# Kernel tuning notes

Hardware: AMD Instinct MI355X
Metric: run time of the kernel (lower is better)

## Reference

```python
import jax, jax.numpy as jnp
import numpy as np

ALPHA = 0.1
K = 10


def setup_inputs() -> dict:
    key = jax.random.key(0)
    k1, k2, k3, k4, k5, k6 = jax.random.split(key, 6)
    N, F_in, H = 100000, 256, 128
    E, E_lp = 1600000, 400000
    return {
        "x": jax.random.normal(k1, (N, F_in), dtype=jnp.float32),
        "edge_index": jax.random.randint(k2, (2, E), 0, N, dtype=jnp.int64),
        "pos_edge_index": jax.random.randint(k3, (2, E_lp), 0, N, dtype=jnp.int64),
        "neg_edge_index": jax.random.randint(k4, (2, E_lp), 0, N, dtype=jnp.int64),
        "W1": jax.random.normal(k5, (F_in, H), dtype=jnp.float32) * (1.0 / np.sqrt(F_in)),
        "W2": jax.random.normal(k6, (H, H), dtype=jnp.float32) * (1.0 / np.sqrt(H)),
    }


def _appnp_propagate(h, src, dst, norm, num_nodes):
    # z_{k+1} = (1-alpha) * A_hat z_k + alpha * h   (K hops)
    z = h
    for _ in range(K):
        msg = norm[:, None] * z[src]                         # [E+N, d] gather
        agg = jax.ops.segment_sum(msg, dst, num_segments=num_nodes)  # scatter-add
        z = (1.0 - ALPHA) * agg + ALPHA * h
    return z


def reference(x, edge_index, pos_edge_index, neg_edge_index, W1, W2):
    N = x.shape[0]
    # add self-loops, GCN symmetric normalization: d^-1/2 A_sl d^-1/2
    loops = jnp.arange(N, dtype=edge_index.dtype)
    src = jnp.concatenate([edge_index[0], loops])
    dst = jnp.concatenate([edge_index[1], loops])
    deg = jax.ops.segment_sum(jnp.ones_like(dst, dtype=x.dtype), dst, num_segments=N)
    dinv = jax.lax.rsqrt(jnp.maximum(deg, 1.0))
    norm = dinv[src] * dinv[dst]

    # encode: two APPNP layers with ReLU in between (drop_rate = 0)
    z = _appnp_propagate(x @ W1, src, dst, norm, N)
    z = jax.nn.relu(z)
    z = _appnp_propagate(z @ W2, src, dst, norm, N)

    # decode: edge dot products over concatenated pos/neg edges
    e = jnp.concatenate([pos_edge_index, neg_edge_index], axis=-1)
    return jnp.sum(z[e[0]] * z[e[1]], axis=-1)
```

## Files before the change

kernel.cpp:

```cpp
#include <hip/hip_runtime.h>


constexpr int Hd = 128;
constexpr int Fin = 256;
constexpr float A_ = 0.1f;
constexpr float OMA = 0.9f;

typedef float vf2 __attribute__((ext_vector_type(2)));
typedef __bf16 bf16x8 __attribute__((ext_vector_type(8)));
typedef float f32x4 __attribute__((ext_vector_type(4)));

__device__ __forceinline__ int idx_at(const void* p, size_t i, int is64) {
    if (is64) return (int)((const long long*)p)[i];
    return ((const int*)p)[i];
}

__device__ __forceinline__ unsigned short bf16_of(float x) {
    unsigned u = __float_as_uint(x);
    return (unsigned short)((u + 0x7fffu + ((u >> 16) & 1u)) >> 16);
}

__device__ __forceinline__ unsigned pack_bf16x2(float x, float y) {
    unsigned ux = __float_as_uint(x);
    unsigned uy = __float_as_uint(y);
    ux = (ux + 0x7fffu + ((ux >> 16) & 1u)) >> 16;
    uy = (uy + 0x7fffu + ((uy >> 16) & 1u)) & 0xffff0000u;
    return ux | uy;
}

__device__ __forceinline__ float2 unpack_bf16x2(unsigned v) {
    float2 r;
    r.x = __uint_as_float(v << 16);
    r.y = __uint_as_float(v & 0xffff0000u);
    return r;
}

__device__ __forceinline__ unsigned short pack_fp8x2(float x, float y) {
    int v = __builtin_amdgcn_cvt_pk_fp8_f32(x, y, 0, false);
    return (unsigned short)(unsigned)v;
}

__device__ __forceinline__ float2 unpack_fp8x2(unsigned short v) {
    vf2 r = __builtin_amdgcn_cvt_pk_f32_fp8((int)(unsigned)v, false);
    float2 o;
    o.x = r[0];
    o.y = r[1];
    return o;
}

__global__ void k_detect(const int* __restrict__ p, int npairs, int* __restrict__ flag) {
    __shared__ int any32;
    if (threadIdx.x == 0) any32 = 0;
    __syncthreads();
    for (int i = threadIdx.x; i < npairs; i += blockDim.x)
        if (p[2 * i + 1] != 0) any32 = 1;
    __syncthreads();
    if (threadIdx.x == 0) *flag = any32 ? 0 : 1;
}


__global__ void k_zero_i32(int* __restrict__ p, int n) {
    int i = blockIdx.x * blockDim.x + threadIdx.x;
    if (i < n) p[i] = 0;
}

__global__ void k_count(const void* __restrict__ ei, int E, int* __restrict__ cnt,
                        const int* __restrict__ flag) {
    int is64 = *flag;
    int e = blockIdx.x * blockDim.x + threadIdx.x;
    if (e < E) {
        int d = idx_at(ei, (size_t)E + e, is64);
        atomicAdd(&cnt[d], 1);
    }
}

__global__ void k_dinv(const int* __restrict__ cnt, float* __restrict__ dinv, int N) {
    int i = blockIdx.x * blockDim.x + threadIdx.x;
    if (i < N) dinv[i] = rsqrtf((float)(cnt[i] + 1));
}

__global__ void k_scan1(const int* __restrict__ cnt, int* __restrict__ rp,
                        int* __restrict__ bsum, int N) {
    __shared__ int s[256];
    int t = threadIdx.x;
    int i = blockIdx.x * 256 + t;
    int v = (i < N) ? (cnt[i] + 1) : 0;
    s[t] = v;
    __syncthreads();
    for (int off = 1; off < 256; off <<= 1) {
        int add = (t >= off) ? s[t - off] : 0;
        __syncthreads();
        s[t] += add;
        __syncthreads();
    }
    if (i < N) rp[i] = s[t] - v;
    if (t == 255) bsum[blockIdx.x] = s[255];
}

__global__ void k_scan2(int* __restrict__ bsum, int nb) {
    __shared__ int s[512];
    int t = threadIdx.x;
    int v = (t < nb) ? bsum[t] : 0;
    s[t] = v;
    __syncthreads();
    for (int off = 1; off < 512; off <<= 1) {
        int add = (t >= off) ? s[t - off] : 0;
        __syncthreads();
        s[t] += add;
        __syncthreads();
    }
    if (t < nb) bsum[t] = s[t] - v;
}

__global__ void k_scan3(int* __restrict__ rp, const int* __restrict__ bsum,
                        int* __restrict__ cursor, int* __restrict__ col,
                        int N, int Etot) {
    int i = blockIdx.x * blockDim.x + threadIdx.x;
    if (i < N) {
        int r = rp[i] + bsum[i >> 8];
        rp[i] = r;
        cursor[i] = 1;
        col[r] = i;
    }
    if (i == 0) rp[N] = Etot;
}

__global__ __launch_bounds__(256) void k_place(const void* __restrict__ ei, int E,
                                               const int* __restrict__ rp,
                                               int* __restrict__ cursor,
                                               int* __restrict__ col,
                                               const int* __restrict__ flag) {
    const int is64 = *flag;
    const int e0 = (blockIdx.x * blockDim.x + threadIdx.x) * 4;
    if (e0 >= E) return;
    const int n = min(4, E - e0);
    int s[4], d[4];
#pragma unroll
    for (int k = 0; k < 4; ++k) {
        int e = e0 + min(k, n - 1);
        s[k] = idx_at(ei, (size_t)e, is64);
        d[k] = idx_at(ei, (size_t)E + e, is64);
    }
    int pos[4];
#pragma unroll
    for (int k = 0; k < 4; ++k)
        if (k < n) pos[k] = rp[d[k]] + atomicAdd(&cursor[d[k]], 1);
#pragma unroll
    for (int k = 0; k < 4; ++k)
        if (k < n) col[pos[k]] = s[k];
}

__global__ void k_wt(const float* __restrict__ W, unsigned short* __restrict__ Wt, int K) {
    int i = blockIdx.x * blockDim.x + threadIdx.x;
    if (i < K * 128) {
        int k = i >> 7, c = i & 127;
        Wt[c * K + k] = bf16_of(W[i]);
    }
}


template <int KTOT, bool AF32>
__global__ __launch_bounds__(256) void k_gemm_mfma(const void* __restrict__ Ap,
                                                   const unsigned short* __restrict__ Wt,
                                                   const float* __restrict__ dinv,
                                                   unsigned short* __restrict__ z0,
                                                   unsigned* __restrict__ ah, int N) {
    __shared__ __align__(16) char smem[64 * 132 * 4];
    unsigned short (*As)[40] = (unsigned short(*)[40])smem;
    unsigned short (*Bs)[40] = (unsigned short(*)[40])(smem + 5120);
    float (*Cs)[132] = (float(*)[132])smem;

    const int t    = threadIdx.x;
    const int lane = t & 63;
    const int w    = t >> 6;
    const int wr   = w >> 1;
    const int wc   = w & 1;
    const int r0   = blockIdx.x * 64;

    f32x4 acc[2][4];
#pragma unroll
    for (int i = 0; i < 2; ++i)
#pragma unroll
        for (int j = 0; j < 4; ++j)
#pragma unroll
            for (int q = 0; q < 4; ++q) acc[i][j][q] = 0.f;

    const int arow = t >> 2;
    const int akc  = (t & 3) * 8;
    const int bcol = t >> 1;
    const int bkc  = (t & 1) * 16;

    for (int k0 = 0; k0 < KTOT; k0 += 32) {
        {
            int gr = r0 + arow;
            if (AF32) {
                uint4 s = make_uint4(0, 0, 0, 0);
                if (gr < N) {
                    const float* a = (const float*)Ap + (size_t)gr * KTOT + k0 + akc;
                    float4 v0 = *(const float4*)a;
                    float4 v1 = *(const float4*)(a + 4);
                    s.x = pack_bf16x2(v0.x, v0.y);
                    s.y = pack_bf16x2(v0.z, v0.w);
                    s.z = pack_bf16x2(v1.x, v1.y);
                    s.w = pack_bf16x2(v1.z, v1.w);
                }
                *(uint4*)&As[arow][akc] = s;
            } else {
                uint4 s = make_uint4(0, 0, 0, 0);
                if (gr < N) s = *(const uint4*)((const unsigned short*)Ap + (size_t)gr * KTOT + k0 + akc);
                *(uint4*)&As[arow][akc] = s;
            }
        }
        {
            const unsigned short* wsrc = Wt + (size_t)bcol * KTOT + k0 + bkc;
            *(uint4*)&Bs[bcol][bkc]     = *(const uint4*)wsrc;
            *(uint4*)&Bs[bcol][bkc + 8] = *(const uint4*)(wsrc + 8);
        }
        __syncthreads();
        {
            const int kblk = (lane >> 4) * 8;
            const int l15  = lane & 15;
            bf16x8 af[2], bfr[4];
#pragma unroll
            for (int i = 0; i < 2; ++i)
                af[i] = *(const bf16x8*)&As[wr * 32 + i * 16 + l15][kblk];
#pragma unroll
            for (int j = 0; j < 4; ++j)
                bfr[j] = *(const bf16x8*)&Bs[wc * 64 + j * 16 + l15][kblk];
#pragma unroll
            for (int i = 0; i < 2; ++i)
#pragma unroll
                for (int j = 0; j < 4; ++j)
                    acc[i][j] = __builtin_amdgcn_mfma_f32_16x16x32_bf16(af[i], bfr[j], acc[i][j], 0, 0, 0);
        }
        __syncthreads();
    }

    {
        const int l15 = lane & 15;
        const int rq  = (lane >> 4) * 4;
#pragma unroll
        for (int i = 0; i < 2; ++i)
#pragma unroll
            for (int j = 0; j < 4; ++j)
#pragma unroll
                for (int q = 0; q < 4; ++q)
                    Cs[wr * 32 + i * 16 + rq + q][wc * 64 + j * 16 + l15] = acc[i][j][q];
    }
    __syncthreads();
    {
        const int row = t >> 2;
        const int cb  = (t & 3) * 32;
        const int gr  = r0 + row;
        if (gr < N) {
            float dv = dinv[gr];
            float c[32];
#pragma unroll
            for (int m = 0; m < 8; ++m) {
                float4 v = *(const float4*)&Cs[row][cb + m * 4];
                c[m * 4 + 0] = v.x; c[m * 4 + 1] = v.y; c[m * 4 + 2] = v.z; c[m * 4 + 3] = v.w;
            }
            unsigned pk[8];
#pragma unroll
            for (int m = 0; m < 8; ++m) {
                unsigned lo = (unsigned)pack_fp8x2(dv * c[4 * m + 0], dv * c[4 * m + 1]);
                unsigned hi = (unsigned)pack_fp8x2(dv * c[4 * m + 2], dv * c[4 * m + 3]);
                pk[m] = lo | (hi << 16);
            }
            uint4* zd = (uint4*)&z0[((size_t)gr << 6) + (cb >> 1)];
            zd[0] = make_uint4(pk[0], pk[1], pk[2], pk[3]);
            zd[1] = make_uint4(pk[4], pk[5], pk[6], pk[7]);
            unsigned am[16];
#pragma unroll
            for (int m = 0; m < 16; ++m)
                am[m] = pack_bf16x2(A_ * c[2 * m], A_ * c[2 * m + 1]);
            uint4* ad = (uint4*)&ah[((size_t)gr << 6) + (cb >> 1)];
            ad[0] = make_uint4(am[0],  am[1],  am[2],  am[3]);
            ad[1] = make_uint4(am[4],  am[5],  am[6],  am[7]);
            ad[2] = make_uint4(am[8],  am[9],  am[10], am[11]);
            ad[3] = make_uint4(am[12], am[13], am[14], am[15]);
        }
    }
}


template <int B>
__device__ __forceinline__ void hop_batch(const unsigned short* __restrict__ yb,
                                          const int* __restrict__ col,
                                          int e, int lane,
                                          float& ax, float& ay,
                                          float& bx, float& by) {
    int c[B];
#pragma unroll
    for (int k = 0; k < B; ++k) c[k] = col[e + k];
    unsigned short v[B];
#pragma unroll
    for (int k = 0; k < B; ++k) v[k] = yb[((unsigned)c[k] << 6) + lane];
#pragma unroll
    for (int k = 0; k < B; ++k) {
        float2 z = unpack_fp8x2(v[k]);
        if (k & 1) { bx += z.x; by += z.y; }
        else       { ax += z.x; ay += z.y; }
    }
}

template <int OUTM>
__global__ __launch_bounds__(256) void k_hop(const unsigned short* __restrict__ yin,
                                             const unsigned* __restrict__ ah,
                                             const float* __restrict__ dinv,
                                             void* __restrict__ zout,
                                             const int* __restrict__ rp,
                                             const int* __restrict__ col, int N) {
    int wid  = (blockIdx.x * blockDim.x + threadIdx.x) >> 6;
    int lane = threadIdx.x & 63;
    if (wid >= N) return;

    int e   = __builtin_amdgcn_readfirstlane(rp[wid]);
    int end = __builtin_amdgcn_readfirstlane(rp[wid + 1]);
    float dv = dinv[wid];

    float2 hh = unpack_bf16x2(ah[((size_t)wid << 6) + lane]);

    float ax = 0.f, ay = 0.f, bx = 0.f, by = 0.f;

    for (; e + 16 <= end; e += 16)
        hop_batch<16>(yin, col, e, lane, ax, ay, bx, by);
    if (e + 8 <= end) { hop_batch<8>(yin, col, e, lane, ax, ay, bx, by); e += 8; }
    if (e + 4 <= end) { hop_batch<4>(yin, col, e, lane, ax, ay, bx, by); e += 4; }
    for (; e < end; ++e) {
        float2 z = unpack_fp8x2(yin[((unsigned)col[e] << 6) + lane]);
        ax += z.x; ay += z.y;
    }

    float q  = OMA * dv;
    float ox = q * (ax + bx) + hh.x;
    float oy = q * (ay + by) + hh.y;
    if (OUTM == 0) {
        ((unsigned short*)zout)[((size_t)wid << 6) + lane] = pack_fp8x2(dv * ox, dv * oy);
    } else if (OUTM == 1) {
        ((unsigned*)zout)[((size_t)wid << 6) + lane] = pack_bf16x2(ox, oy);
    } else {
        ((unsigned*)zout)[((size_t)wid << 6) + lane] =
            pack_bf16x2(fmaxf(ox, 0.f), fmaxf(oy, 0.f));
    }
}


__global__ __launch_bounds__(256) void k_decode(const unsigned* __restrict__ z,
                                                const void* __restrict__ pos,
                                                const void* __restrict__ neg,
                                                float* __restrict__ out, int P, int Q,
                                                const int* __restrict__ flag) {
    int is64 = *flag;
    int t   = blockIdx.x * blockDim.x + threadIdx.x;
    int j   = t >> 4;
    int sub = t & 15;
    if (j >= P + Q) return;
    int a, b;
    if (j < P) { a = idx_at(pos, (size_t)j, is64); b = idx_at(pos, (size_t)P + j, is64); }
    else       { int jj = j - P; a = idx_at(neg, (size_t)jj, is64); b = idx_at(neg, (size_t)Q + jj, is64); }
    const uint4* za = (const uint4*)&z[(size_t)a << 6];
    const uint4* zb = (const uint4*)&z[(size_t)b << 6];
    uint4 va = za[sub];
    uint4 vb = zb[sub];
    float s = 0.f;
    {
        float2 xa, xb;
        xa = unpack_bf16x2(va.x); xb = unpack_bf16x2(vb.x);
        s += xa.x * xb.x + xa.y * xb.y;
        xa = unpack_bf16x2(va.y); xb = unpack_bf16x2(vb.y);
        s += xa.x * xb.x + xa.y * xb.y;
        xa = unpack_bf16x2(va.z); xb = unpack_bf16x2(vb.z);
        s += xa.x * xb.x + xa.y * xb.y;
        xa = unpack_bf16x2(va.w); xb = unpack_bf16x2(vb.w);
        s += xa.x * xb.x + xa.y * xb.y;
    }
#pragma unroll
    for (int off = 8; off >= 1; off >>= 1) s += __shfl_xor(s, off, 16);
    if (sub == 0) out[j] = s;
}


extern "C" void kernel_launch(void* const* d_in, const int* in_sizes, int n_in,
                              void* d_out, int out_size, void* d_ws, size_t ws_size,
                              hipStream_t stream) {
    const float* x   = (const float*)d_in[0];
    const void*  ei  = d_in[1];
    const void*  pos = d_in[2];
    const void*  neg = d_in[3];
    const float* W1  = (const float*)d_in[4];
    const float* W2  = (const float*)d_in[5];
    float*       out = (float*)d_out;

    const int N = in_sizes[0] / Fin;
    const int E = in_sizes[1] / 2;
    const int P = in_sizes[2] / 2;
    const int Q = in_sizes[3] / 2;
    const int Etot = E + N;

    char*  ws  = (char*)d_ws;
    size_t off = 0;
    auto carve = [&](size_t bytes) -> void* {
        void* p = ws + off;
        off = (off + bytes + 511) & ~(size_t)511;
        return p;
    };
    unsigned short* f0   = (unsigned short*)carve((size_t)N * 64 * 2);
    unsigned short* f1   = (unsigned short*)carve((size_t)N * 64 * 2);
    unsigned*       zB2  = (unsigned*)carve((size_t)N * 64 * 4);
    unsigned*       zRB  = (unsigned*)carve((size_t)N * 64 * 4);
    unsigned*       ah   = (unsigned*)carve((size_t)N * 64 * 4);
    unsigned short* Wt1  = (unsigned short*)carve((size_t)128 * 256 * 2);
    unsigned short* Wt2  = (unsigned short*)carve((size_t)128 * 128 * 2);
    float*          dinv = (float*)carve((size_t)N * 4);
    int*     cnt    = (int*)carve((size_t)N * 4);
    int*     rp     = (int*)carve((size_t)(N + 1) * 4);
    int*     cursor = (int*)carve((size_t)N * 4);
    int*     col    = (int*)carve((size_t)Etot * 4);
    int      nb     = (N + 255) / 256;
    int*     bsum   = (int*)carve((size_t)nb * 4);
    int*     flag   = (int*)carve(4);
    (void)ws_size;

    const int gN = (N + 255) / 256;
    const int gE = (E + 255) / 256;

    k_detect<<<1, 256, 0, stream>>>((const int*)ei, 4096, flag);
    k_zero_i32<<<gN, 256, 0, stream>>>(cnt, N);
    k_count<<<gE, 256, 0, stream>>>(ei, E, cnt, flag);
    k_dinv<<<gN, 256, 0, stream>>>(cnt, dinv, N);
    k_scan1<<<nb, 256, 0, stream>>>(cnt, rp, bsum, N);
    k_scan2<<<1, 512, 0, stream>>>(bsum, nb);
    k_scan3<<<gN, 256, 0, stream>>>(rp, bsum, cursor, col, N, Etot);
    k_place<<<(E + 1023) / 1024, 256, 0, stream>>>(ei, E, rp, cursor, col, flag);
    k_wt<<<(256 * 128 + 255) / 256, 256, 0, stream>>>(W1, Wt1, Fin);
    k_wt<<<(128 * 128 + 255) / 256, 256, 0, stream>>>(W2, Wt2, Hd);

    const int gGemm = (N + 63) / 64;
    const int gHop  = (N * 64 + 255) / 256;

    unsigned short* fb[2] = {f0, f1};

    k_gemm_mfma<Fin, true><<<gGemm, 256, 0, stream>>>(x, Wt1, dinv, f0, ah, N);
    for (int k = 0; k < 9; ++k)
        k_hop<0><<<gHop, 256, 0, stream>>>(fb[k & 1], ah, dinv, fb[(k + 1) & 1], rp, col, N);
    k_hop<3><<<gHop, 256, 0, stream>>>(f1, ah, dinv, zRB, rp, col, N);

    k_gemm_mfma<Hd, false><<<gGemm, 256, 0, stream>>>(zRB, Wt2, dinv, f0, ah, N);
    for (int k = 0; k < 9; ++k)
        k_hop<0><<<gHop, 256, 0, stream>>>(fb[k & 1], ah, dinv, fb[(k + 1) & 1], rp, col, N);
    k_hop<1><<<gHop, 256, 0, stream>>>(f1, ah, dinv, zB2, rp, col, N);

    const int gDec = ((P + Q) * 16 + 255) / 256;
    k_decode<<<gDec, 256, 0, stream>>>(zB2, pos, neg, out, P, Q, flag);
}
```

Baseline: 1.042 ms.

## Build CSR via two-pass bucketed binning instead of global atomic placement

Replaces the single edge-placement kernel, which does a global atomicAdd per edge on a random destination cursor, with a bucketed two-pass sort. Edges are histogrammed into buckets of 384 destination nodes, scanned, and scattered into a temporary array, then each bucket places its edges into col using shared-memory cursors. The goal is to swap random global atomics for LDS atomics and more local writes, at the cost of three extra launches and an extra pass over an 8-byte-per-edge temporary buffer. The bucket count is capped at 1024 by the shared arrays and the single-block scan, which limits N to about 393k.

Measured after the change: 1.037 ms. Within noise of the previous version (-0.5%).

```diff
diff --git a/kernel.cpp b/kernel.cpp
--- a/kernel.cpp
+++ b/kernel.cpp
@@ -5,6 +5,7 @@
 constexpr int Fin = 256;
 constexpr float A_ = 0.1f;
 constexpr float OMA = 0.9f;
+constexpr int BSZ = 384;
 
 typedef float vf2 __attribute__((ext_vector_type(2)));
 typedef __bf16 bf16x8 __attribute__((ext_vector_type(8)));
@@ -113,41 +114,103 @@
 }
 
 __global__ void k_scan3(int* __restrict__ rp, const int* __restrict__ bsum,
-                        int* __restrict__ cursor, int* __restrict__ col,
-                        int N, int Etot) {
+                        int* __restrict__ col, int N, int Etot) {
     int i = blockIdx.x * blockDim.x + threadIdx.x;
     if (i < N) {
         int r = rp[i] + bsum[i >> 8];
         rp[i] = r;
-        cursor[i] = 1;
         col[r] = i;
     }
     if (i == 0) rp[N] = Etot;
 }
 
-__global__ __launch_bounds__(256) void k_place(const void* __restrict__ ei, int E,
-                                               const int* __restrict__ rp,
-                                               int* __restrict__ cursor,
-                                               int* __restrict__ col,
-                                               const int* __restrict__ flag) {
-    const int is64 = *flag;
-    const int e0 = (blockIdx.x * blockDim.x + threadIdx.x) * 4;
-    if (e0 >= E) return;
-    const int n = min(4, E - e0);
-    int s[4], d[4];
-#pragma unroll
-    for (int k = 0; k < 4; ++k) {
-        int e = e0 + min(k, n - 1);
-        s[k] = idx_at(ei, (size_t)e, is64);
-        d[k] = idx_at(ei, (size_t)E + e, is64);
-    }
-    int pos[4];
+
+__global__ __launch_bounds__(256) void k_bhist(const void* __restrict__ ei, int E,
+                                               int* __restrict__ bcnt,
+                                               const int* __restrict__ flag, int nbk) {
+    __shared__ int h[1024];
+    int is64 = *flag;
+    for (int i = threadIdx.x; i < nbk; i += 256) h[i] = 0;
+    __syncthreads();
+    for (int e = blockIdx.x * 256 + threadIdx.x; e < E; e += gridDim.x * 256) {
+        int d = idx_at(ei, (size_t)E + e, is64);
+        atomicAdd(&h[d / BSZ], 1);
+    }
+    __syncthreads();
+    for (int i = threadIdx.x; i < nbk; i += 256)
+        if (h[i]) atomicAdd(&bcnt[i], h[i]);
+}
+
+__global__ void k_bscan(const int* __restrict__ bcnt, int* __restrict__ bbase,
+                        int* __restrict__ gcur, int nbk, int E) {
+    __shared__ int s[1024];
+    int t = threadIdx.x;
+    int v = (t < nbk) ? bcnt[t] : 0;
+    s[t] = v;
+    __syncthreads();
+    for (int off = 1; off < 1024; off <<= 1) {
+        int add = (t >= off) ? s[t - off] : 0;
+        __syncthreads();
+        s[t] += add;
+        __syncthreads();
+    }
+    if (t < nbk) {
+        bbase[t] = s[t] - v;
+        gcur[t]  = s[t] - v;
+    }
+    if (t == 0) bbase[nbk] = E;
+}
+
+__global__ __launch_bounds__(256) void k_binA(const void* __restrict__ ei, int E,
+                                              int* __restrict__ gcur,
+                                              int2* __restrict__ tmp,
+                                              const int* __restrict__ flag, int nbk) {
+    __shared__ int hA[1024], hB[1024], sbase[1024];
+    int is64 = *flag;
+    for (int i = threadIdx.x; i < nbk; i += 256) { hA[i] = 0; hB[i] = 0; }
+    __syncthreads();
+    const int e0 = (blockIdx.x * 256 + threadIdx.x) * 4;
+    int s[4], d[4], b[4];
+    const int n = (e0 < E) ? min(4, E - e0) : 0;
 #pragma unroll
     for (int k = 0; k < 4; ++k)
-        if (k < n) pos[k] = rp[d[k]] + atomicAdd(&cursor[d[k]], 1);
+        if (k < n) {
+            s[k] = idx_at(ei, (size_t)(e0 + k), is64);
+            d[k] = idx_at(ei, (size_t)E + (e0 + k), is64);
+            b[k] = d[k] / BSZ;
+            atomicAdd(&hA[b[k]], 1);
+        }
+    __syncthreads();
+    for (int i = threadIdx.x; i < nbk; i += 256)
+        sbase[i] = hA[i] ? atomicAdd(&gcur[i], hA[i]) : 0;
+    __syncthreads();
 #pragma unroll
     for (int k = 0; k < 4; ++k)
-        if (k < n) col[pos[k]] = s[k];
+        if (k < n) {
+            int off = atomicAdd(&hB[b[k]], 1);
+            int2 p;
+            p.x = s[k];
+            p.y = d[k];
+            tmp[sbase[b[k]] + off] = p;
+        }
+}
+
+__global__ __launch_bounds__(256) void k_binB(const int2* __restrict__ tmp,
+                                              const int* __restrict__ bbase,
+                                              const int* __restrict__ rp,
+                                              int* __restrict__ col, int N) {
+    __shared__ int lcur[BSZ];
+    const int b  = blockIdx.x;
+    const int lo = b * BSZ;
+    const int cnt = min(BSZ, N - lo);
+    for (int i = threadIdx.x; i < cnt; i += 256) lcur[i] = 1;
+    __syncthreads();
+    const int start = bbase[b], end = bbase[b + 1];
+    for (int i = start + threadIdx.x; i < end; i += 256) {
+        int2 p = tmp[i];
+        int off = atomicAdd(&lcur[p.y - lo], 1);
+        col[rp[p.y] + off] = p.x;
+    }
 }
 
 __global__ void k_wt(const float* __restrict__ W, unsigned short* __restrict__ Wt, int K) {
@@ -397,6 +460,7 @@
     const int P = in_sizes[2] / 2;
     const int Q = in_sizes[3] / 2;
     const int Etot = E + N;
+    const int nbk  = (N + BSZ - 1) / BSZ;
 
     char*  ws  = (char*)d_ws;
     size_t off = 0;
@@ -415,8 +479,11 @@
     float*          dinv = (float*)carve((size_t)N * 4);
     int*     cnt    = (int*)carve((size_t)N * 4);
     int*     rp     = (int*)carve((size_t)(N + 1) * 4);
-    int*     cursor = (int*)carve((size_t)N * 4);
     int*     col    = (int*)carve((size_t)Etot * 4);
+    int2*    tmp    = (int2*)carve((size_t)E * 8);
+    int*     bcnt   = (int*)carve((size_t)nbk * 4);
+    int*     bbase  = (int*)carve((size_t)(nbk + 1) * 4);
+    int*     gcur   = (int*)carve((size_t)nbk * 4);
     int      nb     = (N + 255) / 256;
     int*     bsum   = (int*)carve((size_t)nb * 4);
     int*     flag   = (int*)carve(4);
@@ -427,12 +494,16 @@
 
     k_detect<<<1, 256, 0, stream>>>((const int*)ei, 4096, flag);
     k_zero_i32<<<gN, 256, 0, stream>>>(cnt, N);
+    k_zero_i32<<<(nbk + 255) / 256, 256, 0, stream>>>(bcnt, nbk);
     k_count<<<gE, 256, 0, stream>>>(ei, E, cnt, flag);
     k_dinv<<<gN, 256, 0, stream>>>(cnt, dinv, N);
     k_scan1<<<nb, 256, 0, stream>>>(cnt, rp, bsum, N);
     k_scan2<<<1, 512, 0, stream>>>(bsum, nb);
-    k_scan3<<<gN, 256, 0, stream>>>(rp, bsum, cursor, col, N, Etot);
-    k_place<<<(E + 1023) / 1024, 256, 0, stream>>>(ei, E, rp, cursor, col, flag);
+    k_scan3<<<gN, 256, 0, stream>>>(rp, bsum, col, N, Etot);
+    k_bhist<<<512, 256, 0, stream>>>(ei, E, bcnt, flag, nbk);
+    k_bscan<<<1, 1024, 0, stream>>>(bcnt, bbase, gcur, nbk, E);
+    k_binA<<<(E + 1023) / 1024, 256, 0, stream>>>(ei, E, gcur, tmp, flag, nbk);
+    k_binB<<<nbk, 256, 0, stream>>>(tmp, bbase, rp, col, N);
     k_wt<<<(256 * 128 + 255) / 256, 256, 0, stream>>>(W1, Wt1, Fin);
     k_wt<<<(128 * 128 + 255) / 256, 256, 0, stream>>>(W2, Wt2, Hd);
 
```
